# Kernel optimization log

Hardware: AMD Instinct MI355X
Metric: run time of the kernel (lower is better)

Reference implementation:

```python
import jax, jax.numpy as jnp
import numpy as np

EPS = 1e-5

def layer_norm(x, alpha, beta):
    mean = jnp.mean(x, axis=-1, keepdims=True)
    var = jnp.mean(jnp.square(x - mean), axis=-1, keepdims=True)
    return alpha * ((x - mean) / jnp.sqrt(var + EPS)) + beta

def setup_inputs() -> dict:
    key = jax.random.key(0)
    B, S, D, H = 4, 2048, 1024, 16
    Dff = 4 * D
    ks = jax.random.split(key, 8)
    inp = {
        "x": jax.random.normal(ks[0], (B, S, D), jnp.float32),
        "attention_mask": jnp.ones((B, S), jnp.int32),
        "ln1_alpha": jnp.ones((D,), jnp.float32),
        "ln1_beta": jnp.zeros((D,), jnp.float32),
        "ln2_alpha": jnp.ones((D,), jnp.float32),
        "ln2_beta": jnp.zeros((D,), jnp.float32),
        "Wq": jax.random.normal(ks[1], (D, D), jnp.float32) * 0.05,
        "Wk": jax.random.normal(ks[2], (D, D), jnp.float32) * 0.05,
        "Wv": jax.random.normal(ks[3], (D, D), jnp.float32) * 0.05,
        "Wo": jax.random.normal(ks[4], (D, D), jnp.float32) * 0.05,
        "W1": jax.random.normal(ks[5], (D, Dff), jnp.float32) * 0.02,
        "b1": jnp.zeros((Dff,), jnp.float32),
        "W2": jax.random.normal(ks[6], (Dff, D), jnp.float32) * 0.02,
        "b2": jnp.zeros((D,), jnp.float32),
    }
    return inp

def reference(x, attention_mask, ln1_alpha, ln1_beta, ln2_alpha, ln2_beta,
              Wq, Wk, Wv, Wo, W1, b1, W2, b2):
    B, S, D = x.shape
    H = 16
    dh = D // H

    # LN1 + self-attention
    y = layer_norm(x, ln1_alpha, ln1_beta)
    Q = (y @ Wq).reshape(B, S, H, dh).transpose(0, 2, 1, 3)  # [B,H,S,dh]
    K = (y @ Wk).reshape(B, S, H, dh).transpose(0, 2, 1, 3)
    V = (y @ Wv).reshape(B, S, H, dh).transpose(0, 2, 1, 3)

    scores = jnp.einsum("bhqd,bhkd->bhqk", Q, K) / jnp.sqrt(jnp.float32(dh))
    causal = jnp.tril(jnp.ones((S, S), jnp.float32))  # [S,S]
    tmask = attention_mask.astype(jnp.float32)  # [B,S]
    amask = causal[None, None, :, :] * tmask[:, None, None, :] * tmask[:, None, :, None]
    scores = jnp.where(amask > 0, scores, jnp.float32(-1e30))
    attn = jax.nn.softmax(scores, axis=-1)
    # dropout omitted (deterministic inference)
    ctx = jnp.einsum("bhqk,bhkd->bhqd", attn, V)
    ctx = ctx.transpose(0, 2, 1, 3).reshape(B, S, D)
    x = x + ctx @ Wo

    # LN2 + GELU FFN
    y = layer_norm(x, ln2_alpha, ln2_beta)
    h = jax.nn.gelu(y @ W1 + b1, approximate=False)
    x = x + (h @ W2 + b2)
    return x
```

## Files before the change

### kernel.cpp

```cpp
#include <hip/hip_runtime.h>
#include <math.h>

typedef unsigned short u16;
typedef unsigned int u32;
typedef __attribute__((ext_vector_type(4))) unsigned short u16x4;
typedef __attribute__((ext_vector_type(8))) short bf16x8;
typedef __attribute__((ext_vector_type(4))) float f32x4;

#define B_ 4
#define S_ 2048
#define D_ 1024
#define H_ 16
#define NT (B_*S_)
#define DFF 4096

static __device__ __forceinline__ float bf2f(u16 u) {
    return __uint_as_float(((u32)u) << 16);
}
static __device__ __forceinline__ u16 f2bf(float f) {
    u32 u = __float_as_uint(f);
    u32 r = (u + 0x7fffu + ((u >> 16) & 1u)) >> 16;
    return (u16)r;
}
static __device__ __forceinline__ void gload_lds16(const void* g, void* l) {
    __builtin_amdgcn_global_load_lds(
        (const __attribute__((address_space(1))) void*)g,
        (__attribute__((address_space(3))) void*)l, 16, 0, 0);
}
static __device__ __forceinline__ float gelu_fast(float x) {
    float x2 = x * x;
    float u = x * fmaf(0.044715f, x2, 1.0f);
    float e = exp2f(2.3022079f * u);
    float r = __builtin_amdgcn_rcpf(e + 1.0f);
    return x - x * r;
}

__global__ void transpose_f2b4(const float* __restrict__ s0, const float* __restrict__ s1,
                               const float* __restrict__ s2, const float* __restrict__ s3,
                               u16* __restrict__ d0, u16* __restrict__ d1,
                               u16* __restrict__ d2, u16* __restrict__ d3,
                               int R, int C) {
    const float* in = s0; u16* out = d0;
    if (blockIdx.z == 1) { in = s1; out = d1; }
    else if (blockIdx.z == 2) { in = s2; out = d2; }
    else if (blockIdx.z == 3) { in = s3; out = d3; }
    __shared__ float t[32][33];
    int c0 = blockIdx.x * 32, r0 = blockIdx.y * 32;
    int x = threadIdx.x, y = threadIdx.y;
    #pragma unroll
    for (int i = 0; i < 4; i++)
        t[y + i*8][x] = in[(long)(r0 + y + i*8) * C + c0 + x];
    __syncthreads();
    #pragma unroll
    for (int i = 0; i < 4; i++)
        out[(long)(c0 + y + i*8) * R + r0 + x] = f2bf(t[x][y + i*8]);
}

__global__ void transpose_f2b(const float* __restrict__ in, u16* __restrict__ out,
                              int R, int C) {
    __shared__ float t[32][33];
    int c0 = blockIdx.x * 32, r0 = blockIdx.y * 32;
    int x = threadIdx.x, y = threadIdx.y;
    #pragma unroll
    for (int i = 0; i < 4; i++)
        t[y + i*8][x] = in[(long)(r0 + y + i*8) * C + c0 + x];
    __syncthreads();
    #pragma unroll
    for (int i = 0; i < 4; i++)
        out[(long)(c0 + y + i*8) * R + r0 + x] = f2bf(t[x][y + i*8]);
}

__global__ void transpose_v(const u16* __restrict__ V, u16* __restrict__ Vt) {
    __shared__ u16 t[32][33];
    int z = blockIdx.z; int b = z >> 4, h = z & 15;
    int s0 = blockIdx.x * 32, d0 = blockIdx.y * 32;
    int x = threadIdx.x, y = threadIdx.y;
    const u16* in = V + ((long)b * S_ + s0) * D_ + h * 64 + d0;
    #pragma unroll
    for (int i = 0; i < 4; i++)
        t[y + i*8][x] = in[(long)(y + i*8) * D_ + x];
    __syncthreads();
    u16* out = Vt + ((long)z * 64 + d0) * S_ + s0;
    #pragma unroll
    for (int i = 0; i < 4; i++)
        out[(long)(y + i*8) * S_ + x] = t[x][y + i*8];
}

__global__ __launch_bounds__(256) void ln_kernel(
    const float* __restrict__ X, const float* __restrict__ alpha,
    const float* __restrict__ beta, u16* __restrict__ Y) {
    int row = blockIdx.x, tid = threadIdx.x;
    float4 xv = ((const float4*)(X + (long)row * D_))[tid];
    float v[4] = {xv.x, xv.y, xv.z, xv.w};
    float s = 0.f, ss = 0.f;
    #pragma unroll
    for (int i = 0; i < 4; i++) { s += v[i]; ss += v[i]*v[i]; }
    #pragma unroll
    for (int off = 32; off >= 1; off >>= 1) {
        s += __shfl_xor(s, off);
        ss += __shfl_xor(ss, off);
    }
    __shared__ float red[8];
    __shared__ float stats[2];
    int w = tid >> 6;
    if ((tid & 63) == 0) { red[w] = s; red[4 + w] = ss; }
    __syncthreads();
    if (tid == 0) {
        float S = red[0] + red[1] + red[2] + red[3];
        float SS = red[4] + red[5] + red[6] + red[7];
        float mean = S * (1.f / D_);
        float var = SS * (1.f / D_) - mean * mean;
        stats[0] = mean; stats[1] = rsqrtf(var + 1e-5f);
    }
    __syncthreads();
    float mean = stats[0], rstd = stats[1];
    float4 av = ((const float4*)alpha)[tid];
    float4 bv = ((const float4*)beta)[tid];
    u16x4 o;
    o[0] = f2bf((v[0] - mean) * rstd * av.x + bv.x);
    o[1] = f2bf((v[1] - mean) * rstd * av.y + bv.y);
    o[2] = f2bf((v[2] - mean) * rstd * av.z + bv.z);
    o[3] = f2bf((v[3] - mean) * rstd * av.w + bv.w);
    *(u16x4*)(Y + (long)row * D_ + tid * 4) = o;
}

#define BM 128
#define BN 128
#define BK 64

__global__ __launch_bounds__(256, 3) void gemm_bt(
    const u16* __restrict__ A,
    const u16* __restrict__ Bt0, const u16* __restrict__ Bt1, const u16* __restrict__ Bt2,
    void* __restrict__ C0, void* __restrict__ C1, void* __restrict__ C2,
    int M, int N, int K, int mode,
    const float* __restrict__ bias, const float* __restrict__ resid) {
    const u16* Bt = Bt0; void* C = C0;
    if (blockIdx.z == 1) { Bt = Bt1; C = C1; }
    else if (blockIdx.z == 2) { Bt = Bt2; C = C2; }

    __shared__ __align__(16) u16 Asm[BM * BK];
    __shared__ __align__(16) u16 Bsm[BN * BK];

    int tid = threadIdx.x;
    int lane = tid & 63, wave = tid >> 6;
    int l15 = lane & 15, quad = lane >> 4;
    int wm = wave & 1, wn = wave >> 1;
    long tm0 = (long)blockIdx.y * BM, tn0 = (long)blockIdx.x * BN;

    int srow = lane >> 3;
    int scol = (lane & 7) * 8;

    f32x4 acc[4][4] = {};

    for (int k0 = 0; k0 < K; k0 += BK) {
        __syncthreads();
        #pragma unroll
        for (int c = 0; c < 4; c++) {
            int chunk = wave * 4 + c;
            int row = chunk * 8 + srow;
            gload_lds16(&A[(tm0 + row) * (long)K + k0 + scol], &Asm[chunk * 512]);
            gload_lds16(&Bt[(tn0 + row) * (long)K + k0 + scol], &Bsm[chunk * 512]);
        }
        __syncthreads();
        #pragma unroll
        for (int ks = 0; ks < 2; ks++) {
            bf16x8 af[4], bfm[4];
            #pragma unroll
            for (int mt = 0; mt < 4; mt++)
                af[mt] = *(const bf16x8*)&Asm[(wm*64 + mt*16 + l15) * BK + ks*32 + quad*8];
            #pragma unroll
            for (int nt = 0; nt < 4; nt++)
                bfm[nt] = *(const bf16x8*)&Bsm[(wn*64 + nt*16 + l15) * BK + ks*32 + quad*8];
            #pragma unroll
            for (int mt = 0; mt < 4; mt++)
                #pragma unroll
                for (int nt = 0; nt < 4; nt++)
                    acc[mt][nt] = __builtin_amdgcn_mfma_f32_16x16x32_bf16(
                        af[mt], bfm[nt], acc[mt][nt], 0, 0, 0);
        }
    }

    #pragma unroll
    for (int mt = 0; mt < 4; mt++) {
        #pragma unroll
        for (int nt = 0; nt < 4; nt++) {
            #pragma unroll
            for (int i = 0; i < 4; i++) {
                long r = tm0 + wm*64 + mt*16 + quad*4 + i;
                long cn = tn0 + wn*64 + nt*16 + l15;
                long idx = r * N + cn;
                float val = acc[mt][nt][i];
                if (mode == 0) {
                    ((u16*)C)[idx] = f2bf(val);
                } else if (mode == 1) {
                    ((float*)C)[idx] = val + resid[idx];
                } else if (mode == 2) {
                    val += bias[cn];
                    val = 0.5f * val * (1.0f + erff(val * 0.70710678118654752f));
                    ((u16*)C)[idx] = f2bf(val);
                } else {
                    ((float*)C)[idx] = val + bias[cn] + resid[idx];
                }
            }
        }
    }
}

#define BM2 256
#define BN2 256
#define BK2 64

__global__ __launch_bounds__(512, 2) void gemm256(
    const u16* __restrict__ A,
    const u16* __restrict__ Bt0, const u16* __restrict__ Bt1, const u16* __restrict__ Bt2,
    void* __restrict__ C0, void* __restrict__ C1, void* __restrict__ C2,
    int M, int N, int K, int mode, const float* __restrict__ bias) {
    const u16* Bt = Bt0; void* C = C0;
    if (blockIdx.z == 1) { Bt = Bt1; C = C1; }
    else if (blockIdx.z == 2) { Bt = Bt2; C = C2; }

    __shared__ __align__(16) u16 Asm[BM2 * BK2];
    __shared__ __align__(16) u16 Bsm[BN2 * BK2];

    int tid = threadIdx.x;
    int lane = tid & 63, wave = tid >> 6;
    int l15 = lane & 15, quad = lane >> 4;
    int wm = wave & 1, wn = wave >> 1;
    long tm0 = (long)blockIdx.y * BM2, tn0 = (long)blockIdx.x * BN2;

    int srow = lane >> 3;
    int scol = (lane & 7) * 8;

    f32x4 acc[8][4] = {};

    for (int k0 = 0; k0 < K; k0 += BK2) {
        __syncthreads();
        #pragma unroll
        for (int c = 0; c < 4; c++) {
            int chunk = wave * 4 + c;
            int row = chunk * 8 + srow;
            gload_lds16(&A[(tm0 + row) * (long)K + k0 + scol], &Asm[chunk * 512]);
            gload_lds16(&Bt[(tn0 + row) * (long)K + k0 + scol], &Bsm[chunk * 512]);
        }
        __syncthreads();
        #pragma unroll
        for (int ks = 0; ks < 2; ks++) {
            bf16x8 af[8], bfm[4];
            #pragma unroll
            for (int mt = 0; mt < 8; mt++)
                af[mt] = *(const bf16x8*)&Asm[(wm*128 + mt*16 + l15) * BK2 + ks*32 + quad*8];
            #pragma unroll
            for (int nt = 0; nt < 4; nt++)
                bfm[nt] = *(const bf16x8*)&Bsm[(wn*64 + nt*16 + l15) * BK2 + ks*32 + quad*8];
            #pragma unroll
            for (int mt = 0; mt < 8; mt++)
                #pragma unroll
                for (int nt = 0; nt < 4; nt++)
                    acc[mt][nt] = __builtin_amdgcn_mfma_f32_16x16x32_bf16(
                        af[mt], bfm[nt], acc[mt][nt], 0, 0, 0);
        }
    }

    #pragma unroll
    for (int mt = 0; mt < 8; mt++) {
        #pragma unroll
        for (int nt = 0; nt < 4; nt++) {
            #pragma unroll
            for (int i = 0; i < 4; i++) {
                long r = tm0 + wm*128 + mt*16 + quad*4 + i;
                long cn = tn0 + wn*64 + nt*16 + l15;
                long idx = r * N + cn;
                float val = acc[mt][nt][i];
                if (mode == 0) {
                    ((u16*)C)[idx] = f2bf(val);
                } else {
                    val += bias[cn];
                    ((u16*)C)[idx] = f2bf(gelu_fast(val));
                }
            }
        }
    }
}

#define LDP 72

__global__ __launch_bounds__(256, 2) void attn_kernel(
    const u16* __restrict__ Q, const u16* __restrict__ Kg, const u16* __restrict__ Vt,
    const int* __restrict__ mask, u16* __restrict__ O) {
    __shared__ __align__(16) u16 Psm[4][32 * LDP];
    int tid = threadIdx.x;
    int lane = tid & 63, wave = tid >> 6;
    int l15 = lane & 15, quad = lane >> 4;
    int bh = blockIdx.x; int b = bh >> 4, h = bh & 15;
    int y = blockIdx.y;
    long tokBase = (long)b * S_;
    const float SCL = 0.125f * 1.4426950408889634f;
    const float MMAX = 20.0f;

    const bf16x8 ones = {16256,16256,16256,16256,16256,16256,16256,16256};
    u16* Pw = Psm[wave];
    const int* mb = mask + b * S_;

    int t;
    if (wave == 0)      t = y;
    else if (wave == 1) t = 63 - y;
    else if (wave == 2) t = 31 - y;
    else                t = 32 + y;
    int q0 = t * 32;

    bf16x8 aq[2][2];
    #pragma unroll
    for (int mt = 0; mt < 2; mt++) {
        const u16* qptr = Q + (tokBase + q0 + mt*16 + l15) * D_ + h * 64;
        aq[mt][0] = *(const bf16x8*)(qptr + quad * 8);
        aq[mt][1] = *(const bf16x8*)(qptr + 32 + quad * 8);
    }

    f32x4 o[2][4] = {};
    f32x4 lacc[2] = {};
    int ktiles = t / 2 + 1;

    for (int kt = 0; kt < ktiles; kt++) {
        int k0 = kt * 64;
        bf16x8 kb[4][2], vb[4][2];
        #pragma unroll
        for (int nt = 0; nt < 4; nt++) {
            const u16* kp = Kg + (tokBase + k0 + nt*16 + l15) * D_ + h * 64;
            kb[nt][0] = *(const bf16x8*)(kp + quad * 8);
            kb[nt][1] = *(const bf16x8*)(kp + 32 + quad * 8);
        }
        #pragma unroll
        for (int d = 0; d < 4; d++) {
            const u16* vp = Vt + ((long)bh * 64 + d*16 + l15) * S_ + k0;
            vb[d][0] = *(const bf16x8*)(vp + quad * 8);
            vb[d][1] = *(const bf16x8*)(vp + 32 + quad * 8);
        }

        f32x4 s[2][4] = {};
        #pragma unroll
        for (int nt = 0; nt < 4; nt++) {
            s[0][nt] = __builtin_amdgcn_mfma_f32_16x16x32_bf16(aq[0][0], kb[nt][0], s[0][nt], 0,0,0);
            s[0][nt] = __builtin_amdgcn_mfma_f32_16x16x32_bf16(aq[0][1], kb[nt][1], s[0][nt], 0,0,0);
            s[1][nt] = __builtin_amdgcn_mfma_f32_16x16x32_bf16(aq[1][0], kb[nt][0], s[1][nt], 0,0,0);
            s[1][nt] = __builtin_amdgcn_mfma_f32_16x16x32_bf16(aq[1][1], kb[nt][1], s[1][nt], 0,0,0);
        }

        int mk = 0;
        #pragma unroll
        for (int nt = 0; nt < 4; nt++)
            if (mb[k0 + nt*16 + l15] != 0) mk |= (1 << nt);

        #pragma unroll
        for (int mt = 0; mt < 2; mt++) {
            #pragma unroll
            for (int i = 0; i < 4; i++) {
                int qq = q0 + mt*16 + quad*4 + i;
                #pragma unroll
                for (int nt = 0; nt < 4; nt++) {
                    int kc = k0 + nt*16 + l15;
                    float p = exp2f(fmaf(s[mt][nt][i], SCL, -MMAX));
                    p = (kc <= qq && ((mk >> nt) & 1)) ? p : 0.f;
                    Pw[(mt*16 + quad*4 + i) * LDP + nt*16 + l15] = f2bf(p);
                }
            }
        }
        asm volatile("s_waitcnt lgkmcnt(0)" ::: "memory");

        #pragma unroll
        for (int hv = 0; hv < 2; hv++) {
            bf16x8 ap0 = *(const bf16x8*)&Pw[l15 * LDP + hv*32 + quad*8];
            bf16x8 ap1 = *(const bf16x8*)&Pw[(16 + l15) * LDP + hv*32 + quad*8];
            #pragma unroll
            for (int d = 0; d < 4; d++) {
                o[0][d] = __builtin_amdgcn_mfma_f32_16x16x32_bf16(ap0, vb[d][hv], o[0][d], 0,0,0);
                o[1][d] = __builtin_amdgcn_mfma_f32_16x16x32_bf16(ap1, vb[d][hv], o[1][d], 0,0,0);
            }
            lacc[0] = __builtin_amdgcn_mfma_f32_16x16x32_bf16(ap0, ones, lacc[0], 0,0,0);
            lacc[1] = __builtin_amdgcn_mfma_f32_16x16x32_bf16(ap1, ones, lacc[1], 0,0,0);
        }
    }

    #pragma unroll
    for (int mt = 0; mt < 2; mt++) {
        #pragma unroll
        for (int i = 0; i < 4; i++) {
            float inv = 1.f / lacc[mt][i];
            long r = tokBase + q0 + mt*16 + quad*4 + i;
            #pragma unroll
            for (int d = 0; d < 4; d++)
                O[r * D_ + h*64 + d*16 + l15] = f2bf(o[mt][d][i] * inv);
        }
    }
}

extern "C" void kernel_launch(void* const* d_in, const int* in_sizes, int n_in,
                              void* d_out, int out_size, void* d_ws, size_t ws_size,
                              hipStream_t stream) {
    const float* x    = (const float*)d_in[0];
    const int*   am   = (const int*)d_in[1];
    const float* ln1a = (const float*)d_in[2];
    const float* ln1b = (const float*)d_in[3];
    const float* ln2a = (const float*)d_in[4];
    const float* ln2b = (const float*)d_in[5];
    const float* wq   = (const float*)d_in[6];
    const float* wk   = (const float*)d_in[7];
    const float* wv   = (const float*)d_in[8];
    const float* wo   = (const float*)d_in[9];
    const float* w1   = (const float*)d_in[10];
    const float* b1   = (const float*)d_in[11];
    const float* w2   = (const float*)d_in[12];
    const float* b2   = (const float*)d_in[13];
    float* out = (float*)d_out;

    char* ws = (char*)d_ws;
    const size_t MB16 = (size_t)16 * 1024 * 1024;
    u16* y1      = (u16*)(ws + 0 * MB16);
    u16* q       = (u16*)(ws + 1 * MB16);
    u16* k       = (u16*)(ws + 2 * MB16);
    u16* v       = (u16*)(ws + 3 * MB16);
    u16* wqt     = (u16*)(ws + 4 * MB16 + 0 * (size_t)D_ * D_ * 2);
    u16* wkt     = (u16*)(ws + 4 * MB16 + 1 * (size_t)D_ * D_ * 2);
    u16* wvt     = (u16*)(ws + 4 * MB16 + 2 * (size_t)D_ * D_ * 2);
    u16* wot     = (u16*)(ws + 4 * MB16 + 3 * (size_t)D_ * D_ * 2);
    u16* y2      = y1;
    u16* w1t     = q;
    u16* w2t     = q + (size_t)D_ * DFF;
    u16* h_full  = k;
    u16* ctx     = v;
    u16*   vt  = (u16*)d_out;
    float* x1f = out;

    dim3 tb(32, 8);
    transpose_f2b4<<<dim3(D_/32, D_/32, 4), tb, 0, stream>>>(
        wq, wk, wv, wo, wqt, wkt, wvt, wot, D_, D_);

    ln_kernel<<<NT, 256, 0, stream>>>(x, ln1a, ln1b, y1);

    gemm256<<<dim3(D_/BN2, NT/BM2, 3), 512, 0, stream>>>(
        y1, wqt, wkt, wvt, q, k, v, NT, D_, D_, 0, nullptr);

    transpose_v<<<dim3(S_/32, 2, B_*H_), tb, 0, stream>>>(v, vt);

    attn_kernel<<<dim3(B_*H_, 16), 256, 0, stream>>>(q, k, vt, am, ctx);

    gemm_bt<<<dim3(D_/BN, NT/BM, 1), 256, 0, stream>>>(
        ctx, wot, wot, wot, x1f, x1f, x1f, NT, D_, D_, 1, nullptr, x);

    transpose_f2b<<<dim3(DFF/32, D_/32), tb, 0, stream>>>(w1, w1t, D_, DFF);
    transpose_f2b<<<dim3(D_/32, DFF/32), tb, 0, stream>>>(w2, w2t, DFF, D_);

    ln_kernel<<<NT, 256, 0, stream>>>(x1f, ln2a, ln2b, y2);

    gemm256<<<dim3(DFF/BN2, NT/BM2, 1), 512, 0, stream>>>(
        y2, w1t, w1t, w1t, h_full, h_full, h_full, NT, DFF, D_, 2, b1);
    gemm_bt<<<dim3(D_/BN, NT/BM, 1), 256, 0, stream>>>(
        h_full, w2t, w2t, w2t, out, out, out, NT, D_, DFF, 3, b2, x1f);
}
```

Before: 696.6 us.

## Double-buffer the 256x256 GEMM with phased prefetch and merge QKV into one weight matrix

Replaces gemm256 with gemm8p, a GEMM with a double-buffered LDS ring. It splits each K-step into four MFMA phases, each interleaved with async global-to-LDS loads for later tiles, separated by raw barriers, with s_setprio raised during MFMA bursts. This is meant to hide global load latency behind matrix math instead of stalling on a sync every K-step. The QKV projection now treats the contiguous transposed Wq/Wk/Wv as one N=3072 weight and routes output columns to q/k/v in the epilogue. The cost is 128KB of LDS per block, which likely cuts residency to one block per CU, and fragile hand-written vmcnt accounting.

Result: faster. 676.3 us (-2.9%).

```diff
diff --git a/kernel.cpp b/kernel.cpp
--- a/kernel.cpp
+++ b/kernel.cpp
@@ -34,6 +34,10 @@
     float r = __builtin_amdgcn_rcpf(e + 1.0f);
     return x - x * r;
 }
+
+#define MBAR() do { asm volatile("" ::: "memory"); \
+                    __builtin_amdgcn_s_barrier(); \
+                    asm volatile("" ::: "memory"); } while (0)
 
 __global__ void transpose_f2b4(const float* __restrict__ s0, const float* __restrict__ s1,
                                const float* __restrict__ s2, const float* __restrict__ s3,
@@ -196,8 +200,7 @@
                     ((float*)C)[idx] = val + resid[idx];
                 } else if (mode == 2) {
                     val += bias[cn];
-                    val = 0.5f * val * (1.0f + erff(val * 0.70710678118654752f));
-                    ((u16*)C)[idx] = f2bf(val);
+                    ((u16*)C)[idx] = f2bf(gelu_fast(val));
                 } else {
                     ((float*)C)[idx] = val + bias[cn] + resid[idx];
                 }
@@ -210,55 +213,128 @@
 #define BN2 256
 #define BK2 64
 
-__global__ __launch_bounds__(512, 2) void gemm256(
-    const u16* __restrict__ A,
-    const u16* __restrict__ Bt0, const u16* __restrict__ Bt1, const u16* __restrict__ Bt2,
-    void* __restrict__ C0, void* __restrict__ C1, void* __restrict__ C2,
-    int M, int N, int K, int mode, const float* __restrict__ bias) {
-    const u16* Bt = Bt0; void* C = C0;
-    if (blockIdx.z == 1) { Bt = Bt1; C = C1; }
-    else if (blockIdx.z == 2) { Bt = Bt2; C = C2; }
-
-    __shared__ __align__(16) u16 Asm[BM2 * BK2];
-    __shared__ __align__(16) u16 Bsm[BN2 * BK2];
+__global__ __launch_bounds__(512, 2) void gemm8p(
+    const u16* __restrict__ A, const u16* __restrict__ Bt,
+    u16* __restrict__ C0, u16* __restrict__ C1, u16* __restrict__ C2,
+    int N, int K, int mode, const float* __restrict__ bias) {
+    __shared__ __align__(16) u16 lds[2 * 32768];
 
     int tid = threadIdx.x;
     int lane = tid & 63, wave = tid >> 6;
     int l15 = lane & 15, quad = lane >> 4;
     int wm = wave & 1, wn = wave >> 1;
     long tm0 = (long)blockIdx.y * BM2, tn0 = (long)blockIdx.x * BN2;
-
     int srow = lane >> 3;
     int scol = (lane & 7) * 8;
+    int steps = K >> 6;
+
+    auto STAGE = [&](int kt, int half, int buf) {
+        long kk = (long)kt * BK2;
+        #pragma unroll
+        for (int c = 0; c < 2; c++) {
+            int chunk = wave * 2 + c;
+            int rloc = (half & 1) * 128 + chunk * 8 + srow;
+            const u16* g = (half < 2)
+                ? &A [(tm0 + rloc) * (long)K + kk + scol]
+                : &Bt[(tn0 + rloc) * (long)K + kk + scol];
+            u16* l = &lds[buf * 32768 + (half >= 2 ? 16384 : 0)
+                          + (half & 1) * 8192 + chunk * 512];
+            gload_lds16(g, l);
+        }
+    };
 
     f32x4 acc[8][4] = {};
-
-    for (int k0 = 0; k0 < K; k0 += BK2) {
-        __syncthreads();
-        #pragma unroll
-        for (int c = 0; c < 4; c++) {
-            int chunk = wave * 4 + c;
-            int row = chunk * 8 + srow;
-            gload_lds16(&A[(tm0 + row) * (long)K + k0 + scol], &Asm[chunk * 512]);
-            gload_lds16(&Bt[(tn0 + row) * (long)K + k0 + scol], &Bsm[chunk * 512]);
-        }
-        __syncthreads();
-        #pragma unroll
-        for (int ks = 0; ks < 2; ks++) {
-            bf16x8 af[8], bfm[4];
-            #pragma unroll
-            for (int mt = 0; mt < 8; mt++)
-                af[mt] = *(const bf16x8*)&Asm[(wm*128 + mt*16 + l15) * BK2 + ks*32 + quad*8];
-            #pragma unroll
-            for (int nt = 0; nt < 4; nt++)
-                bfm[nt] = *(const bf16x8*)&Bsm[(wn*64 + nt*16 + l15) * BK2 + ks*32 + quad*8];
-            #pragma unroll
-            for (int mt = 0; mt < 8; mt++)
-                #pragma unroll
-                for (int nt = 0; nt < 4; nt++)
-                    acc[mt][nt] = __builtin_amdgcn_mfma_f32_16x16x32_bf16(
-                        af[mt], bfm[nt], acc[mt][nt], 0, 0, 0);
-        }
+    bf16x8 af[4][2], bl[2][2], bh[2][2];
+
+    STAGE(0, 0, 0); STAGE(0, 1, 0); STAGE(0, 2, 0); STAGE(0, 3, 0);
+    if (steps > 1) { STAGE(1, 2, 1); STAGE(1, 3, 1); }
+    if (steps > 1) asm volatile("s_waitcnt vmcnt(4)" ::: "memory");
+    else           asm volatile("s_waitcnt vmcnt(0)" ::: "memory");
+    MBAR();
+
+    for (int t = 0; t < steps; ++t) {
+        int cur = t & 1;
+        const u16* Ab = &lds[cur * 32768];
+        const u16* Bb = &lds[cur * 32768 + 16384];
+        bool pf1 = (t + 1 < steps), pf2 = (t + 2 < steps);
+
+        #pragma unroll
+        for (int mt = 0; mt < 4; mt++) {
+            const u16* p = &Ab[(wm*128 + mt*16 + l15) * BK2];
+            af[mt][0] = *(const bf16x8*)(p + quad*8);
+            af[mt][1] = *(const bf16x8*)(p + 32 + quad*8);
+        }
+        #pragma unroll
+        for (int nt = 0; nt < 2; nt++) {
+            const u16* p = &Bb[(wn*64 + nt*16 + l15) * BK2];
+            bl[nt][0] = *(const bf16x8*)(p + quad*8);
+            bl[nt][1] = *(const bf16x8*)(p + 32 + quad*8);
+        }
+        if (pf1) STAGE(t + 1, 0, cur ^ 1);
+        MBAR();
+        __builtin_amdgcn_s_setprio(1);
+        #pragma unroll
+        for (int mt = 0; mt < 4; mt++)
+            #pragma unroll
+            for (int nt = 0; nt < 2; nt++) {
+                acc[mt][nt] = __builtin_amdgcn_mfma_f32_16x16x32_bf16(af[mt][0], bl[nt][0], acc[mt][nt], 0,0,0);
+                acc[mt][nt] = __builtin_amdgcn_mfma_f32_16x16x32_bf16(af[mt][1], bl[nt][1], acc[mt][nt], 0,0,0);
+            }
+        __builtin_amdgcn_s_setprio(0);
+        MBAR();
+
+        #pragma unroll
+        for (int nt = 0; nt < 2; nt++) {
+            const u16* p = &Bb[(wn*64 + (2+nt)*16 + l15) * BK2];
+            bh[nt][0] = *(const bf16x8*)(p + quad*8);
+            bh[nt][1] = *(const bf16x8*)(p + 32 + quad*8);
+        }
+        if (pf1) STAGE(t + 1, 1, cur ^ 1);
+        MBAR();
+        __builtin_amdgcn_s_setprio(1);
+        #pragma unroll
+        for (int mt = 0; mt < 4; mt++)
+            #pragma unroll
+            for (int nt = 0; nt < 2; nt++) {
+                acc[mt][2+nt] = __builtin_amdgcn_mfma_f32_16x16x32_bf16(af[mt][0], bh[nt][0], acc[mt][2+nt], 0,0,0);
+                acc[mt][2+nt] = __builtin_amdgcn_mfma_f32_16x16x32_bf16(af[mt][1], bh[nt][1], acc[mt][2+nt], 0,0,0);
+            }
+        __builtin_amdgcn_s_setprio(0);
+        MBAR();
+
+        #pragma unroll
+        for (int mt = 0; mt < 4; mt++) {
+            const u16* p = &Ab[(wm*128 + 64 + mt*16 + l15) * BK2];
+            af[mt][0] = *(const bf16x8*)(p + quad*8);
+            af[mt][1] = *(const bf16x8*)(p + 32 + quad*8);
+        }
+        if (pf2) STAGE(t + 2, 2, cur);
+        MBAR();
+        __builtin_amdgcn_s_setprio(1);
+        #pragma unroll
+        for (int mt = 0; mt < 4; mt++)
+            #pragma unroll
+            for (int nt = 0; nt < 2; nt++) {
+                acc[4+mt][2+nt] = __builtin_amdgcn_mfma_f32_16x16x32_bf16(af[mt][0], bh[nt][0], acc[4+mt][2+nt], 0,0,0);
+                acc[4+mt][2+nt] = __builtin_amdgcn_mfma_f32_16x16x32_bf16(af[mt][1], bh[nt][1], acc[4+mt][2+nt], 0,0,0);
+            }
+        __builtin_amdgcn_s_setprio(0);
+        MBAR();
+
+        if (pf2) STAGE(t + 2, 3, cur);
+        MBAR();
+        __builtin_amdgcn_s_setprio(1);
+        #pragma unroll
+        for (int mt = 0; mt < 4; mt++)
+            #pragma unroll
+            for (int nt = 0; nt < 2; nt++) {
+                acc[4+mt][nt] = __builtin_amdgcn_mfma_f32_16x16x32_bf16(af[mt][0], bl[nt][0], acc[4+mt][nt], 0,0,0);
+                acc[4+mt][nt] = __builtin_amdgcn_mfma_f32_16x16x32_bf16(af[mt][1], bl[nt][1], acc[4+mt][nt], 0,0,0);
+            }
+        __builtin_amdgcn_s_setprio(0);
+        if (pf2) asm volatile("s_waitcnt vmcnt(4)" ::: "memory");
+        else     asm volatile("s_waitcnt vmcnt(0)" ::: "memory");
+        MBAR();
     }
 
     #pragma unroll
@@ -268,14 +344,16 @@
             #pragma unroll
             for (int i = 0; i < 4; i++) {
                 long r = tm0 + wm*128 + mt*16 + quad*4 + i;
-                long cn = tn0 + wn*64 + nt*16 + l15;
-                long idx = r * N + cn;
+                int cn = (int)tn0 + wn*64 + nt*16 + l15;
                 float val = acc[mt][nt][i];
                 if (mode == 0) {
-                    ((u16*)C)[idx] = f2bf(val);
+                    int mi = cn >> 10;
+                    int col = cn & 1023;
+                    u16* base = (mi == 0) ? C0 : (mi == 1 ? C1 : C2);
+                    base[r * 1024 + col] = f2bf(val);
                 } else {
                     val += bias[cn];
-                    ((u16*)C)[idx] = f2bf(gelu_fast(val));
+                    C0[r * (long)N + cn] = f2bf(gelu_fast(val));
                 }
             }
         }
@@ -436,8 +514,8 @@
 
     ln_kernel<<<NT, 256, 0, stream>>>(x, ln1a, ln1b, y1);
 
-    gemm256<<<dim3(D_/BN2, NT/BM2, 3), 512, 0, stream>>>(
-        y1, wqt, wkt, wvt, q, k, v, NT, D_, D_, 0, nullptr);
+    gemm8p<<<dim3(3*D_/BN2, NT/BM2), 512, 0, stream>>>(
+        y1, wqt, q, k, v, 3*D_, D_, 0, nullptr);
 
     transpose_v<<<dim3(S_/32, 2, B_*H_), tb, 0, stream>>>(v, vt);
 
@@ -451,8 +529,8 @@
 
     ln_kernel<<<NT, 256, 0, stream>>>(x1f, ln2a, ln2b, y2);
 
-    gemm256<<<dim3(DFF/BN2, NT/BM2, 1), 512, 0, stream>>>(
-        y2, w1t, w1t, w1t, h_full, h_full, h_full, NT, DFF, D_, 2, b1);
+    gemm8p<<<dim3(DFF/BN2, NT/BM2), 512, 0, stream>>>(
+        y2, w1t, h_full, h_full, h_full, DFF, D_, 2, b1);
     gemm_bt<<<dim3(D_/BN, NT/BM, 1), 256, 0, stream>>>(
         h_full, w2t, w2t, w2t, out, out, out, NT, D_, DFF, 3, b2, x1f);
 }
```
